# Kernel optimization log

Measured on AMD Instinct MI355X. Metric: run time of the kernel, lower is better.

The kernel has to match this reference:

```python
import jax, jax.numpy as jnp
import numpy as np

# corner enumeration order matches the original list comprehension:
# (0,0,0),(0,0,d),(0,h,0),(0,h,d),(w,0,0),(w,0,d),(w,h,0),(w,h,d)
CORNER_OFFS = jnp.array([[0,0,0],[0,0,1],[0,1,0],[0,1,1],
                         [1,0,0],[1,0,1],[1,1,0],[1,1,1]], dtype=jnp.float32)
# axis_combinations in original: (i,j) with j>=i over 3 axes -> 6 combos
CROSS_A = jnp.array([0,0,0,1,1,2])
CROSS_B = jnp.array([0,1,2,1,2,2])


def setup_inputs() -> dict:
    key = jax.random.key(0)
    k1, k2, k3 = jax.random.split(key, 3)
    B = 1024
    bb = jax.random.uniform(k1, (B, 6), dtype=jnp.float32)
    rotations = jax.random.normal(k2, (B, 3, 3), dtype=jnp.float32)
    translations = jax.random.normal(k3, (B, 1, 3), dtype=jnp.float32)
    return {"bb": bb, "rotations": rotations, "translations": translations}


def _pv_loss(bb, rotations, translations):
    B = bb.shape[0]
    # [B,8,3] axis-aligned corners, then rotate (corners @ R) and translate
    corners = bb[:, None, :3] + bb[:, None, 3:] * CORNER_OFFS
    corners_t = jnp.einsum('bkd,bde->bke', corners, rotations) + translations
    # unit_vectors is the 3x3 identity, so I @ R == R
    uvt = rotations  # [B,3,3] rows are the transformed unit vectors

    ii, jj = jnp.triu_indices(B, k=1)  # all pairs j > i, P = B(B-1)/2
    c1 = corners_t[ii]  # [P,8,3]
    c2 = corners_t[jj]  # [P,8,3]
    u1 = uvt[ii]        # [P,3,3]
    u2 = uvt[jj]        # [P,3,3]

    # NOTE: the original second axis-loop also uses unit_vector_first[i]
    # (a bug we replicate): the 3 face axes of the FIRST box are tested twice;
    # duplicates do not change min() or the all-intersect decision, so we test
    # them once. Cross axes use the j>=i combinations.
    face_axes = u1                                           # [P,3,3]
    cross_axes = jnp.cross(u1[:, CROSS_A, :], u2[:, CROSS_B, :])  # [P,6,3]
    axes = jnp.concatenate([face_axes, cross_axes], axis=1)  # [P,9,3]
    # original skips exactly-zero cross axes (torch.equal with zeros)
    valid = jnp.concatenate(
        [jnp.ones(face_axes.shape[:2], dtype=bool),
         jnp.any(cross_axes != 0, axis=-1)], axis=1)         # [P,9]

    # SAT projections: dot every corner with every axis
    d1 = jnp.einsum('pkc,pac->pak', c1, axes)  # [P,9,8]
    d2 = jnp.einsum('pkc,pac->pak', c2, axes)  # [P,9,8]
    min1, max1 = d1.min(-1), d1.max(-1)
    min2, max2 = d2.min(-1), d2.max(-1)
    total_len = jnp.maximum(max1, max2) - jnp.minimum(min1, min2)
    sum_len = (max1 - min1) + (max2 - min2)
    overlap = sum_len - total_len                 # [P,9]

    axis_pass = jnp.where(valid, total_len < sum_len, True)
    pair_pass = jnp.all(axis_pass, axis=-1)       # [P]
    overlap_masked = jnp.where(valid, overlap, jnp.inf)
    penalty = jnp.where(pair_pass, overlap_masked.min(-1), 0.0)
    return penalty.sum()


def reference(bb, rotations, translations):
    return _pv_loss(bb, rotations, translations)
```

## Files before the change

### kernel.cpp

```cpp
#include <hip/hip_runtime.h>
#include <hip/hip_bf16.h>

#define NI 2
#define JT 256

__device__ __forceinline__ void load_box(const float* __restrict__ bb,
                                         const float* __restrict__ rot,
                                         const float* __restrict__ tr,
                                         int b, float* R, float* c, float* e) {
    const float* s = bb + b * 6;
    const float* r = rot + b * 9;
    const float* t = tr + b * 3;
    float d0 = s[3], d1 = s[4], d2 = s[5];
    float a0 = s[0] + 0.5f * d0, a1 = s[1] + 0.5f * d1, a2 = s[2] + 0.5f * d2;
#pragma unroll
    for (int k = 0; k < 9; k++) R[k] = r[k];
#pragma unroll
    for (int k = 0; k < 3; k++) {
        c[k]     = a0 * R[k] + a1 * R[3 + k] + a2 * R[6 + k] + t[k];
        e[k]     = d0 * R[k];
        e[3 + k] = d1 * R[3 + k];
        e[6 + k] = d2 * R[6 + k];
    }
}

__device__ __forceinline__ float axis_overlap(float ax, float ay, float az,
                                              const float* ci, const float* ei,
                                              const float* cj, const float* ej) {
    float s1 = ci[0] * ax + ci[1] * ay + ci[2] * az;
    float u0 = ei[0] * ax + ei[1] * ay + ei[2] * az;
    float u1 = ei[3] * ax + ei[4] * ay + ei[5] * az;
    float u2 = ei[6] * ax + ei[7] * ay + ei[8] * az;
    float h1 = 0.5f * (fabsf(u0) + fabsf(u1) + fabsf(u2));

    float s2 = cj[0] * ax + cj[1] * ay + cj[2] * az;
    float v0 = ej[0] * ax + ej[1] * ay + ej[2] * az;
    float v1 = ej[3] * ax + ej[4] * ay + ej[5] * az;
    float v2 = ej[6] * ax + ej[7] * ay + ej[8] * az;
    float h2 = 0.5f * (fabsf(v0) + fabsf(v1) + fabsf(v2));

    return fminf(s1 + h1, s2 + h2) - fmaxf(s1 - h1, s2 - h2);
}

__global__ __launch_bounds__(JT) void pv_pairs(const float* __restrict__ bb,
                                               const float* __restrict__ rot,
                                               const float* __restrict__ tr,
                                               float* __restrict__ partial, int B) {
    const int icAll = (B + NI - 1) / NI;
    int bid = blockIdx.x;
    int jc = 0, base = 0, ic = 0;
    for (;; jc++) {
        int icmax = min(((jc + 1) * JT + NI - 1) / NI, icAll);
        if (bid < base + icmax) { ic = bid - base; break; }
        base += icmax;
    }
    const int jbase = jc * JT;
    const int ibase = ic * NI;
    const int j = jbase + threadIdx.x;

    float pen = 0.0f;
    if (j < B) {
        float Rj[9], cj[3], ej[9];
        load_box(bb, rot, tr, j, Rj, cj, ej);

#pragma unroll
        for (int ii = 0; ii < NI; ii++) {
            const int i = ibase + ii;
            if (i >= B) break;
            if (i >= j) continue;
            float Ri[9], ci[3], ei[9];
            load_box(bb, rot, tr, i, Ri, ci, ei);

            bool pass = true;
            float minov = __builtin_inff();

#pragma unroll
            for (int a = 0; a < 3; a++) {
                float ov = axis_overlap(Ri[a * 3], Ri[a * 3 + 1], Ri[a * 3 + 2],
                                        ci, ei, cj, ej);
                pass = pass && (ov > 0.0f);
                minov = fminf(minov, ov);
            }
            const int CA[6] = {0, 0, 0, 1, 1, 2};
            const int CB[6] = {0, 1, 2, 1, 2, 2};
#pragma unroll
            for (int cc = 0; cc < 6; cc++) {
                const int ra = CA[cc], rb = CB[cc];
                float ux = Ri[ra * 3], uy = Ri[ra * 3 + 1], uz = Ri[ra * 3 + 2];
                float vx = Rj[rb * 3], vy = Rj[rb * 3 + 1], vz = Rj[rb * 3 + 2];
                float ax = uy * vz - uz * vy;
                float ay = uz * vx - ux * vz;
                float az = ux * vy - uy * vx;
                if ((ax != 0.0f) || (ay != 0.0f) || (az != 0.0f)) {
                    float ov = axis_overlap(ax, ay, az, ci, ei, cj, ej);
                    pass = pass && (ov > 0.0f);
                    minov = fminf(minov, ov);
                }
            }
            pen += pass ? minov : 0.0f;
        }
    }

#pragma unroll
    for (int off = 32; off > 0; off >>= 1) pen += __shfl_down(pen, off);
    __shared__ float wsum[JT / 64];
    const int wid = threadIdx.x >> 6;
    if ((threadIdx.x & 63) == 0) wsum[wid] = pen;
    __syncthreads();
    if (threadIdx.x == 0) {
        float s = 0.0f;
#pragma unroll
        for (int w = 0; w < JT / 64; w++) s += wsum[w];
        partial[blockIdx.x] = s;
    }
}

__global__ __launch_bounds__(256) void pv_reduce(const float* __restrict__ partial,
                                                 float* __restrict__ out, int n) {
    float s = 0.0f;
    for (int k = threadIdx.x; k < n; k += 256) s += partial[k];
#pragma unroll
    for (int off = 32; off > 0; off >>= 1) s += __shfl_down(s, off);
    __shared__ float wsum[4];
    const int wid = threadIdx.x >> 6;
    if ((threadIdx.x & 63) == 0) wsum[wid] = s;
    __syncthreads();
    if (threadIdx.x == 0) out[0] = wsum[0] + wsum[1] + wsum[2] + wsum[3];
}

extern "C" void kernel_launch(void* const* d_in, const int* in_sizes, int n_in,
                              void* d_out, int out_size, void* d_ws, size_t ws_size,
                              hipStream_t stream) {
    const float* bb  = (const float*)d_in[0];
    const float* rot = (const float*)d_in[1];
    const float* tr  = (const float*)d_in[2];
    float* out = (float*)d_out;
    const int B = in_sizes[0] / 6;

    float* partial = (float*)d_ws;

    const int gx = (B + JT - 1) / JT;
    const int icAll = (B + NI - 1) / NI;
    int total = 0;
    for (int jc = 0; jc < gx; jc++) {
        int icmax = ((jc + 1) * JT + NI - 1) / NI;
        total += (icmax < icAll) ? icmax : icAll;
    }

    pv_pairs<<<dim3(total), dim3(JT), 0, stream>>>(bb, rot, tr, partial, B);
    pv_reduce<<<1, 256, 0, stream>>>(partial, out, total);
}
```

Measured before the change: 68.66 us.

## Assign one i-box per block and replace the reduce kernel with atomicAdd

```diff
diff --git a/kernel.cpp b/kernel.cpp
--- a/kernel.cpp
+++ b/kernel.cpp
@@ -1,7 +1,6 @@
 #include <hip/hip_runtime.h>
 #include <hip/hip_bf16.h>
 
-#define NI 2
 #define JT 256
 
 __device__ __forceinline__ void load_box(const float* __restrict__ bb,
@@ -45,60 +44,50 @@
 __global__ __launch_bounds__(JT) void pv_pairs(const float* __restrict__ bb,
                                                const float* __restrict__ rot,
                                                const float* __restrict__ tr,
-                                               float* __restrict__ partial, int B) {
-    const int icAll = (B + NI - 1) / NI;
+                                               float* __restrict__ out, int B) {
     int bid = blockIdx.x;
-    int jc = 0, base = 0, ic = 0;
+    int jc = 0, base = 0, i = 0;
     for (;; jc++) {
-        int icmax = min(((jc + 1) * JT + NI - 1) / NI, icAll);
-        if (bid < base + icmax) { ic = bid - base; break; }
+        int icmax = min((jc + 1) * JT, B);
+        if (bid < base + icmax) { i = bid - base; break; }
         base += icmax;
     }
-    const int jbase = jc * JT;
-    const int ibase = ic * NI;
-    const int j = jbase + threadIdx.x;
+    const int j = jc * JT + threadIdx.x;
 
     float pen = 0.0f;
-    if (j < B) {
+    if (j < B && j > i) {
+        float Ri[9], ci[3], ei[9];
+        load_box(bb, rot, tr, i, Ri, ci, ei);
         float Rj[9], cj[3], ej[9];
         load_box(bb, rot, tr, j, Rj, cj, ej);
 
-#pragma unroll
-        for (int ii = 0; ii < NI; ii++) {
-            const int i = ibase + ii;
-            if (i >= B) break;
-            if (i >= j) continue;
-            float Ri[9], ci[3], ei[9];
-            load_box(bb, rot, tr, i, Ri, ci, ei);
-
-            bool pass = true;
-            float minov = __builtin_inff();
+        bool pass = true;
+        float minov = __builtin_inff();
 
 #pragma unroll
-            for (int a = 0; a < 3; a++) {
-                float ov = axis_overlap(Ri[a * 3], Ri[a * 3 + 1], Ri[a * 3 + 2],
-                                        ci, ei, cj, ej);
+        for (int a = 0; a < 3; a++) {
+            float ov = axis_overlap(Ri[a * 3], Ri[a * 3 + 1], Ri[a * 3 + 2],
+                                    ci, ei, cj, ej);
+            pass = pass && (ov > 0.0f);
+            minov = fminf(minov, ov);
+        }
+        const int CA[6] = {0, 0, 0, 1, 1, 2};
+        const int CB[6] = {0, 1, 2, 1, 2, 2};
+#pragma unroll
+        for (int cc = 0; cc < 6; cc++) {
+            const int ra = CA[cc], rb = CB[cc];
+            float ux = Ri[ra * 3], uy = Ri[ra * 3 + 1], uz = Ri[ra * 3 + 2];
+            float vx = Rj[rb * 3], vy = Rj[rb * 3 + 1], vz = Rj[rb * 3 + 2];
+            float ax = uy * vz - uz * vy;
+            float ay = uz * vx - ux * vz;
+            float az = ux * vy - uy * vx;
+            if ((ax != 0.0f) || (ay != 0.0f) || (az != 0.0f)) {
+                float ov = axis_overlap(ax, ay, az, ci, ei, cj, ej);
                 pass = pass && (ov > 0.0f);
                 minov = fminf(minov, ov);
             }
-            const int CA[6] = {0, 0, 0, 1, 1, 2};
-            const int CB[6] = {0, 1, 2, 1, 2, 2};
-#pragma unroll
-            for (int cc = 0; cc < 6; cc++) {
-                const int ra = CA[cc], rb = CB[cc];
-                float ux = Ri[ra * 3], uy = Ri[ra * 3 + 1], uz = Ri[ra * 3 + 2];
-                float vx = Rj[rb * 3], vy = Rj[rb * 3 + 1], vz = Rj[rb * 3 + 2];
-                float ax = uy * vz - uz * vy;
-                float ay = uz * vx - ux * vz;
-                float az = ux * vy - uy * vx;
-                if ((ax != 0.0f) || (ay != 0.0f) || (az != 0.0f)) {
-                    float ov = axis_overlap(ax, ay, az, ci, ei, cj, ej);
-                    pass = pass && (ov > 0.0f);
-                    minov = fminf(minov, ov);
-                }
-            }
-            pen += pass ? minov : 0.0f;
         }
+        pen = pass ? minov : 0.0f;
     }
 
 #pragma unroll
@@ -111,21 +100,8 @@
         float s = 0.0f;
 #pragma unroll
         for (int w = 0; w < JT / 64; w++) s += wsum[w];
-        partial[blockIdx.x] = s;
+        atomicAdd(out, s);
     }
-}
-
-__global__ __launch_bounds__(256) void pv_reduce(const float* __restrict__ partial,
-                                                 float* __restrict__ out, int n) {
-    float s = 0.0f;
-    for (int k = threadIdx.x; k < n; k += 256) s += partial[k];
-#pragma unroll
-    for (int off = 32; off > 0; off >>= 1) s += __shfl_down(s, off);
-    __shared__ float wsum[4];
-    const int wid = threadIdx.x >> 6;
-    if ((threadIdx.x & 63) == 0) wsum[wid] = s;
-    __syncthreads();
-    if (threadIdx.x == 0) out[0] = wsum[0] + wsum[1] + wsum[2] + wsum[3];
 }
 
 extern "C" void kernel_launch(void* const* d_in, const int* in_sizes, int n_in,
@@ -137,16 +113,14 @@
     float* out = (float*)d_out;
     const int B = in_sizes[0] / 6;
 
-    float* partial = (float*)d_ws;
+    hipMemsetAsync(out, 0, sizeof(float), stream);
 
     const int gx = (B + JT - 1) / JT;
-    const int icAll = (B + NI - 1) / NI;
     int total = 0;
     for (int jc = 0; jc < gx; jc++) {
-        int icmax = ((jc + 1) * JT + NI - 1) / NI;
-        total += (icmax < icAll) ? icmax : icAll;
+        int icmax = (jc + 1) * JT;
+        total += (icmax < B) ? icmax : B;
     }
 
-    pv_pairs<<<dim3(total), dim3(JT), 0, stream>>>(bb, rot, tr, partial, B);
-    pv_reduce<<<1, 256, 0, stream>>>(partial, out, total);
+    pv_pairs<<<dim3(total), dim3(JT), 0, stream>>>(bb, rot, tr, out, B);
 }
```

Measured after the change: 92.97 us. +35.4%, slower.
